# Performance work log

Hardware: AMD Instinct MI355X
Metric: run time of the kernel (lower is better)

Reference implementation:

```python
import jax, jax.numpy as jnp
import numpy as np

CH = 256            # channels
IN_C = CH // 2      # 128
INTER_C = CH // 16  # 16
NUM_POINTS = 32
BN_EPS = 1e-5


def conv1x1(x, W, b=None):
    # x: [B,C,H,W], W: [O,C]
    y = jnp.einsum('oc,bchw->bohw', W, x)
    if b is not None:
        y = y + b[None, :, None, None]
    return y


def bilinear_sample(feat, sx, sy):
    """feat [B,C,H,W]; sx,sy [B,N,P] continuous index coords; border padding."""
    B, C, H, W = feat.shape
    x0f = jnp.floor(sx)
    y0f = jnp.floor(sy)
    wx = sx - x0f
    wy = sy - y0f
    x0 = jnp.clip(x0f.astype(jnp.int32), 0, W - 1)
    x1 = jnp.clip(x0f.astype(jnp.int32) + 1, 0, W - 1)
    y0 = jnp.clip(y0f.astype(jnp.int32), 0, H - 1)
    y1 = jnp.clip(y0f.astype(jnp.int32) + 1, 0, H - 1)
    feat_f = feat.reshape(B, C, H * W).transpose(0, 2, 1)  # [B,HW,C]

    def gather(yi, xi):
        idx = (yi * W + xi).reshape(B, -1)  # [B,N*P]
        return jnp.take_along_axis(feat_f, idx[:, :, None], axis=1)  # [B,N*P,C]

    wxf = wx.reshape(B, -1, 1)
    wyf = wy.reshape(B, -1, 1)
    out = (gather(y0, x0) * (1 - wxf) * (1 - wyf)
           + gather(y0, x1) * wxf * (1 - wyf)
           + gather(y1, x0) * (1 - wxf) * wyf
           + gather(y1, x1) * wxf * wyf)
    N, P = sx.shape[1], sx.shape[2]
    return out.reshape(B, N, P, C)


def multi_scale_attention(qf, vf, Wq, bq, Wk, bk, Wv, bv, Woff, boff):
    # deformable-style point-sampling attention with NUM_POINTS samples per query
    B, _, H, W = qf.shape
    N = H * W
    q = conv1x1(qf, Wq, bq).reshape(B, INTER_C, N).transpose(0, 2, 1)  # [B,N,Ci]
    k = conv1x1(vf, Wk, bk)                                            # [B,Ci,H,W]
    v = conv1x1(vf, Wv, bv)                                            # [B,Cv,H,W]
    off = conv1x1(qf, Woff, boff).reshape(B, NUM_POINTS, 2, N)
    off = off.transpose(0, 3, 1, 2)                                    # [B,N,P,2] (dx,dy)
    ys, xs = jnp.meshgrid(jnp.arange(H, dtype=qf.dtype),
                          jnp.arange(W, dtype=qf.dtype), indexing='ij')
    sx = xs.reshape(-1)[None, :, None] + off[..., 0]                   # [B,N,P]
    sy = ys.reshape(-1)[None, :, None] + off[..., 1]
    k_s = bilinear_sample(k, sx, sy)                                   # [B,N,P,Ci]
    v_s = bilinear_sample(v, sx, sy)                                   # [B,N,P,Cv]
    logits = jnp.einsum('bnc,bnpc->bnp', q, k_s) / jnp.sqrt(jnp.asarray(INTER_C, qf.dtype))
    attn = jax.nn.softmax(logits, axis=-1)
    out = jnp.einsum('bnp,bnpc->bnc', attn, v_s)                       # [B,N,Cv]
    return out.transpose(0, 2, 1).reshape(B, -1, H, W)


def setup_inputs() -> dict:
    key = jax.random.key(0)
    ks = jax.random.split(key, 12)
    B, Hl, Wl, Hh, Wh = 2, 64, 64, 32, 32
    s = 0.02
    return {
        'low_feature': jax.random.normal(ks[0], (B, CH, Hl, Wl), jnp.float32),
        'high_feature': jax.random.normal(ks[1], (B, CH, Hh, Wh), jnp.float32),
        'W1': jax.random.normal(ks[2], (IN_C, 2 * CH), jnp.float32) * s,
        'b1': jnp.zeros((IN_C,), jnp.float32),
        'W2': jax.random.normal(ks[3], (IN_C, CH), jnp.float32) * s,
        'b2': jnp.zeros((IN_C,), jnp.float32),
        'Wq': jax.random.normal(ks[4], (INTER_C, IN_C), jnp.float32) * s,
        'bq': jnp.zeros((INTER_C,), jnp.float32),
        'Wk': jax.random.normal(ks[5], (INTER_C, IN_C), jnp.float32) * s,
        'bk': jnp.zeros((INTER_C,), jnp.float32),
        'Wv': jax.random.normal(ks[6], (IN_C, IN_C), jnp.float32) * s,
        'bv': jnp.zeros((IN_C,), jnp.float32),
        'Woff': jax.random.normal(ks[7], (2 * NUM_POINTS, IN_C), jnp.float32) * 0.5,
        'boff': jnp.zeros((2 * NUM_POINTS,), jnp.float32),
        'Wb': jax.random.normal(ks[8], (CH, IN_C + CH), jnp.float32) * s,
        'gamma': jnp.ones((CH,), jnp.float32),
        'beta': jnp.zeros((CH,), jnp.float32),
        'rmean': jnp.zeros((CH,), jnp.float32),
        'rvar': jnp.ones((CH,), jnp.float32),
    }


def reference(low_feature, high_feature, W1, b1, W2, b2, Wq, bq, Wk, bk,
              Wv, bv, Woff, boff, Wb, gamma, beta, rmean, rvar):
    B, _, Hl, Wl = low_feature.shape
    # F.interpolate(mode='bilinear', align_corners=False) == jax.image half-pixel bilinear
    high_up = jax.image.resize(high_feature, (B, CH, Hl, Wl), method='bilinear')
    query_feature = conv1x1(jnp.concatenate([high_up, low_feature], axis=1), W1, b1)
    value_feature = conv1x1(high_up, W2, b2)
    value_feature = multi_scale_attention(query_feature, value_feature,
                                          Wq, bq, Wk, bk, Wv, bv, Woff, boff)
    x = conv1x1(jnp.concatenate([value_feature, high_up], axis=1), Wb)
    # BatchNorm (eval form) + ReLU
    x = (x - rmean[None, :, None, None]) * jax.lax.rsqrt(rvar + BN_EPS)[None, :, None, None]
    x = x * gamma[None, :, None, None] + beta[None, :, None, None]
    return jax.nn.relu(x)
```

## Files before the change

### kernel.cpp

```cpp
#include <hip/hip_runtime.h>
#include <hip/hip_bf16.h>

#define NL 4096
#define HH 32
#define WH 32

typedef __attribute__((ext_vector_type(8))) short s8v;
typedef __attribute__((ext_vector_type(4))) short s4v;
typedef __attribute__((ext_vector_type(4))) float f32x4;

static __device__ inline unsigned short f2bf(float x) {
  __hip_bfloat16 h = __float2bfloat16(x);
  return *reinterpret_cast<unsigned short*>(&h);
}
static __device__ inline float bfbits2f(unsigned int lo16) {
  unsigned int u = lo16 << 16;
  return *reinterpret_cast<float*>(&u);
}

__global__ __launch_bounds__(256) void convert_weights_k(
    const float* __restrict__ w1, const float* __restrict__ w2,
    const float* __restrict__ wq, const float* __restrict__ woff,
    const float* __restrict__ wk, const float* __restrict__ wv,
    const float* __restrict__ wb, short* __restrict__ dst) {
  int i = blockIdx.x * 256 + threadIdx.x;
  const float* src; int off;
  if      (i <  65536) { src = w1;   off = 0; }
  else if (i <  98304) { src = w2;   off = 65536; }
  else if (i < 100352) { src = wq;   off = 98304; }
  else if (i < 108544) { src = woff; off = 100352; }
  else if (i < 110592) { src = wk;   off = 108544; }
  else if (i < 126976) { src = wv;   off = 110592; }
  else if (i < 225280) { src = wb;   off = 126976; }
  else return;
  dst[i] = (short)f2bf(src[i - off]);
}

__global__ __launch_bounds__(256) void k1_fused(
    const float* __restrict__ low, const float* __restrict__ high,
    const short* __restrict__ wc,
    const float* __restrict__ b1, const float* __restrict__ b2,
    const float* __restrict__ bq, const float* __restrict__ boff,
    const float* __restrict__ bk, const float* __restrict__ bv,
    short* __restrict__ xh, float* __restrict__ q_t, float* __restrict__ k_t,
    float* __restrict__ off_t, short* __restrict__ v_t) {
  __shared__ short xin_s[16 * 520];
  __shared__ short qf_s[16 * 136];
  __shared__ short vf_s[16 * 136];
  const int tid = threadIdx.x;
  const int pix0 = blockIdx.x * 16;
  const int b = pix0 >> 12;
  const int n0 = pix0 & (NL - 1);

  {
    const int nl = tid & 15, cg = tid >> 4;
    const int n = n0 + nl;
    const int y = n >> 6, x = n & 63;
    float sx = x * 0.5f - 0.25f;
    float sy = y * 0.5f - 0.25f;
    float x0f = floorf(sx), y0f = floorf(sy);
    float wx = sx - x0f, wy = sy - y0f;
    int x0i = (int)x0f, y0i = (int)y0f;
    int x0c = min(WH - 1, max(0, x0i)), x1c = min(WH - 1, max(0, x0i + 1));
    int y0c = min(HH - 1, max(0, y0i)), y1c = min(HH - 1, max(0, y0i + 1));
    float w00 = (1.f - wy) * (1.f - wx), w01 = (1.f - wy) * wx;
    float w10 = wy * (1.f - wx),         w11 = wy * wx;
#pragma unroll
    for (int i = 0; i < 16; i++) {
      int c = cg * 16 + i;
      const float* f = high + (size_t)(b * 256 + c) * (HH * WH);
      float v = w00 * f[y0c * WH + x0c] + w01 * f[y0c * WH + x1c]
              + w10 * f[y1c * WH + x0c] + w11 * f[y1c * WH + x1c];
      xin_s[nl * 520 + c] = (short)f2bf(v);
      xin_s[nl * 520 + 256 + c] =
          (short)f2bf(low[(size_t)(b * 256 + c) * NL + n]);
    }
  }
  __syncthreads();

  {
    const int r = tid >> 4, c0 = (tid & 15) * 16;
    s8v v0 = *(const s8v*)(xin_s + r * 520 + c0);
    s8v v1 = *(const s8v*)(xin_s + r * 520 + c0 + 8);
    *(s8v*)(xh + (size_t)(pix0 + r) * 256 + c0) = v0;
    *(s8v*)(xh + (size_t)(pix0 + r) * 256 + c0 + 8) = v1;
  }

  const int wave = tid >> 6, lane = tid & 63;
  const int quad = lane >> 4, id = lane & 15;

  {
    f32x4 acc0 = (f32x4){0.f, 0.f, 0.f, 0.f};
    f32x4 acc1 = (f32x4){0.f, 0.f, 0.f, 0.f};
    const short* a0 = wc + (size_t)(wave * 32 + id) * 512 + quad * 8;
    const short* a1 = a0 + 16 * 512;
    const short* bp = xin_s + id * 520 + quad * 8;
#pragma unroll
    for (int kk = 0; kk < 512; kk += 32) {
      s8v bf = *(const s8v*)(bp + kk);
      acc0 = __builtin_amdgcn_mfma_f32_16x16x32_bf16(*(const s8v*)(a0 + kk), bf, acc0, 0, 0, 0);
      acc1 = __builtin_amdgcn_mfma_f32_16x16x32_bf16(*(const s8v*)(a1 + kk), bf, acc1, 0, 0, 0);
    }
    int m0 = wave * 32 + quad * 4;
    s4v o0, o1;
#pragma unroll
    for (int r = 0; r < 4; r++) {
      o0[r] = (short)f2bf(acc0[r] + b1[m0 + r]);
      o1[r] = (short)f2bf(acc1[r] + b1[m0 + 16 + r]);
    }
    *(s4v*)(qf_s + id * 136 + m0) = o0;
    *(s4v*)(qf_s + id * 136 + m0 + 16) = o1;
  }

  {
    f32x4 acc0 = (f32x4){0.f, 0.f, 0.f, 0.f};
    f32x4 acc1 = (f32x4){0.f, 0.f, 0.f, 0.f};
    const short* a0 = wc + 65536 + (size_t)(wave * 32 + id) * 256 + quad * 8;
    const short* a1 = a0 + 16 * 256;
    const short* bp = xin_s + id * 520 + quad * 8;
#pragma unroll
    for (int kk = 0; kk < 256; kk += 32) {
      s8v bf = *(const s8v*)(bp + kk);
      acc0 = __builtin_amdgcn_mfma_f32_16x16x32_bf16(*(const s8v*)(a0 + kk), bf, acc0, 0, 0, 0);
      acc1 = __builtin_amdgcn_mfma_f32_16x16x32_bf16(*(const s8v*)(a1 + kk), bf, acc1, 0, 0, 0);
    }
    int m0 = wave * 32 + quad * 4;
    s4v o0, o1;
#pragma unroll
    for (int r = 0; r < 4; r++) {
      o0[r] = (short)f2bf(acc0[r] + b2[m0 + r]);
      o1[r] = (short)f2bf(acc1[r] + b2[m0 + 16 + r]);
    }
    *(s4v*)(vf_s + id * 136 + m0) = o0;
    *(s4v*)(vf_s + id * 136 + m0 + 16) = o1;
  }
  __syncthreads();

  for (int f = wave; f < 14; f += 4) {
    const short* ap = wc + 98304 + (size_t)(f * 16 + id) * 128 + quad * 8;
    const short* bp = (f < 5 ? qf_s : vf_s) + id * 136 + quad * 8;
    f32x4 acc = (f32x4){0.f, 0.f, 0.f, 0.f};
#pragma unroll
    for (int kk = 0; kk < 128; kk += 32)
      acc = __builtin_amdgcn_mfma_f32_16x16x32_bf16(
          *(const s8v*)(ap + kk), *(const s8v*)(bp + kk), acc, 0, 0, 0);
    const int pix = pix0 + id;
    const int mq = quad * 4;
    if (f == 0) {
      f32x4 v;
#pragma unroll
      for (int r = 0; r < 4; r++) v[r] = acc[r] + bq[mq + r];
      *(f32x4*)(q_t + (size_t)pix * 16 + mq) = v;
    } else if (f < 5) {
      int m = (f - 1) * 16 + mq;
      f32x4 v;
#pragma unroll
      for (int r = 0; r < 4; r++) v[r] = acc[r] + boff[m + r];
      *(f32x4*)(off_t + (size_t)pix * 64 + m) = v;
    } else if (f == 5) {
      f32x4 v;
#pragma unroll
      for (int r = 0; r < 4; r++) v[r] = acc[r] + bk[mq + r];
      *(f32x4*)(k_t + (size_t)pix * 16 + mq) = v;
    } else {
      int m = (f - 6) * 16 + mq;
      s4v o;
#pragma unroll
      for (int r = 0; r < 4; r++) o[r] = (short)f2bf(acc[r] + bv[m + r]);
      *(s4v*)(v_t + (size_t)pix * 128 + m) = o;
    }
  }
}

__global__ __launch_bounds__(1024, 2) void k2_fused(
    const float* __restrict__ q_t, const float* __restrict__ k_t,
    const short* __restrict__ v_t, const float* __restrict__ off_t,
    const short* __restrict__ xh, const short* __restrict__ wb,
    const float* __restrict__ gamma, const float* __restrict__ beta,
    const float* __restrict__ rmean, const float* __restrict__ rvar,
    float* __restrict__ out) {
  __shared__ float s_w[16][32][4];
  __shared__ int   s_i[16][32][4];
  __shared__ short attn_s[16 * 136];
  const int tid = threadIdx.x;
  const int wave = tid >> 6, lane = tid & 63;
  const int pix0 = blockIdx.x * 16;

  {
    const int qidx = pix0 + wave;
    const int b = qidx >> 12;
    const int n = qidx & (NL - 1);
    const int qy = n >> 6, qx = n & 63;

    const float* qp = q_t + (size_t)qidx * 16;
    float qreg[16];
#pragma unroll
    for (int i = 0; i < 16; i += 4) {
      float4 t = *(const float4*)(qp + i);
      qreg[i] = t.x; qreg[i + 1] = t.y; qreg[i + 2] = t.z; qreg[i + 3] = t.w;
    }

    const int pt = lane >> 1, h = lane & 1;
    float2 dxy = *(const float2*)(off_t + (size_t)qidx * 64 + 2 * pt);
    float sx = (float)qx + dxy.x;
    float sy = (float)qy + dxy.y;
    float x0f = floorf(sx), y0f = floorf(sy);
    float wx = sx - x0f, wy = sy - y0f;
    int x0i = (int)x0f, y0i = (int)y0f;
    int x0 = min(63, max(0, x0i)), x1 = min(63, max(0, x0i + 1));
    int y0 = min(63, max(0, y0i)), y1 = min(63, max(0, y0i + 1));

    int   yr  = h ? y1 : y0;
    float wyr = h ? wy : (1.f - wy);
    int   pa = yr * 64 + x0, pb = yr * 64 + x1;
    float wa = wyr * (1.f - wx), wb_ = wyr * wx;

    const float* kb = k_t + (size_t)b * NL * 16;
    float da = 0.f, db = 0.f;
    {
      const float* ka = kb + (size_t)pa * 16;
      const float* kc = kb + (size_t)pb * 16;
#pragma unroll
      for (int i = 0; i < 16; i += 4) {
        float4 a4 = *(const float4*)(ka + i);
        float4 c4 = *(const float4*)(kc + i);
        da = fmaf(qreg[i], a4.x, da); da = fmaf(qreg[i + 1], a4.y, da);
        da = fmaf(qreg[i + 2], a4.z, da); da = fmaf(qreg[i + 3], a4.w, da);
        db = fmaf(qreg[i], c4.x, db); db = fmaf(qreg[i + 1], c4.y, db);
        db = fmaf(qreg[i + 2], c4.z, db); db = fmaf(qreg[i + 3], c4.w, db);
      }
    }
    float part = wa * da + wb_ * db;
    part += __shfl_xor(part, 1, 64);
    float logit = part * 0.25f;

    float m = logit;
#pragma unroll
    for (int s = 32; s > 0; s >>= 1) m = fmaxf(m, __shfl_xor(m, s, 64));
    float e = __expf(logit - m);
    float ssum = e;
#pragma unroll
    for (int s = 32; s > 0; s >>= 1) ssum += __shfl_xor(ssum, s, 64);
    float a = e * 2.f / ssum;

    s_w[wave][pt][2 * h + 0] = a * wa;
    s_w[wave][pt][2 * h + 1] = a * wb_;
    s_i[wave][pt][2 * h + 0] = pa;
    s_i[wave][pt][2 * h + 1] = pb;

    const int t = lane >> 4, chunk = lane & 15;
    const short* vb = v_t + (size_t)b * NL * 128 + chunk * 8;
    float o[8];
#pragma unroll
    for (int j = 0; j < 8; j++) o[j] = 0.f;
#pragma unroll
    for (int pp = 0; pp < 32; pp++) {
      float w_ = s_w[wave][pp][t];
      int  pix = s_i[wave][pp][t];
      uint4 u = *(const uint4*)(vb + (size_t)pix * 128);
      o[0] = fmaf(w_, bfbits2f(u.x & 0xffffu), o[0]);
      o[1] = fmaf(w_, bfbits2f(u.x >> 16),     o[1]);
      o[2] = fmaf(w_, bfbits2f(u.y & 0xffffu), o[2]);
      o[3] = fmaf(w_, bfbits2f(u.y >> 16),     o[3]);
      o[4] = fmaf(w_, bfbits2f(u.z & 0xffffu), o[4]);
      o[5] = fmaf(w_, bfbits2f(u.z >> 16),     o[5]);
      o[6] = fmaf(w_, bfbits2f(u.w & 0xffffu), o[6]);
      o[7] = fmaf(w_, bfbits2f(u.w >> 16),     o[7]);
    }
#pragma unroll
    for (int j = 0; j < 8; j++) {
      o[j] += __shfl_xor(o[j], 16, 64);
      o[j] += __shfl_xor(o[j], 32, 64);
    }
    if (t == 0) {
      uint4 pk;
      pk.x = (unsigned)f2bf(o[0]) | ((unsigned)f2bf(o[1]) << 16);
      pk.y = (unsigned)f2bf(o[2]) | ((unsigned)f2bf(o[3]) << 16);
      pk.z = (unsigned)f2bf(o[4]) | ((unsigned)f2bf(o[5]) << 16);
      pk.w = (unsigned)f2bf(o[6]) | ((unsigned)f2bf(o[7]) << 16);
      *(uint4*)(attn_s + wave * 136 + chunk * 8) = pk;
    }
  }
  __syncthreads();

  {
    const int quad = lane >> 4, id = lane & 15;
    const int m0 = wave * 16;
    const int pix = pix0 + id;

    f32x4 acc = (f32x4){0.f, 0.f, 0.f, 0.f};
    const short* ap = wb + (size_t)(m0 + id) * 384 + quad * 8;
    const short* bs = attn_s + id * 136 + quad * 8;
    const short* bg = xh + (size_t)pix * 256 + quad * 8;
#pragma unroll
    for (int k = 0; k < 4; k++)
      acc = __builtin_amdgcn_mfma_f32_16x16x32_bf16(
          *(const s8v*)(ap + k * 32), *(const s8v*)(bs + k * 32), acc, 0, 0, 0);
#pragma unroll
    for (int k = 0; k < 8; k++)
      acc = __builtin_amdgcn_mfma_f32_16x16x32_bf16(
          *(const s8v*)(ap + 128 + k * 32), *(const s8v*)(bg + k * 32), acc, 0, 0, 0);

    const int bb = pix >> 12, nlow = pix & (NL - 1);
    const int mbase = m0 + quad * 4;
#pragma unroll
    for (int r = 0; r < 4; r++) {
      int o = mbase + r;
      float s  = gamma[o] * rsqrtf(rvar[o] + 1e-5f);
      float sh = beta[o] - rmean[o] * s;
      out[((size_t)bb * 256 + o) * NL + nlow] = fmaxf(fmaf(acc[r], s, sh), 0.f);
    }
  }
}

extern "C" void kernel_launch(void* const* d_in, const int* in_sizes, int n_in,
                              void* d_out, int out_size, void* d_ws, size_t ws_size,
                              hipStream_t stream) {
  const float* low   = (const float*)d_in[0];
  const float* high  = (const float*)d_in[1];
  const float* W1    = (const float*)d_in[2];
  const float* b1    = (const float*)d_in[3];
  const float* W2    = (const float*)d_in[4];
  const float* b2    = (const float*)d_in[5];
  const float* Wq    = (const float*)d_in[6];
  const float* bq    = (const float*)d_in[7];
  const float* Wk    = (const float*)d_in[8];
  const float* bk    = (const float*)d_in[9];
  const float* Wv    = (const float*)d_in[10];
  const float* bv    = (const float*)d_in[11];
  const float* Woff  = (const float*)d_in[12];
  const float* boff  = (const float*)d_in[13];
  const float* Wb    = (const float*)d_in[14];
  const float* gamma = (const float*)d_in[15];
  const float* beta  = (const float*)d_in[16];
  const float* rmean = (const float*)d_in[17];
  const float* rvar  = (const float*)d_in[18];
  float* out = (float*)d_out;

  short* ws    = (short*)d_ws;
  short* xh    = ws;
  short* v_t   = xh + 2097152;
  short* wc    = v_t + 1048576;
  float* q_t   = (float*)(wc + 225280);
  float* k_t   = q_t + 131072;
  float* off_t = k_t + 131072;

  convert_weights_k<<<880, 256, 0, stream>>>(W1, W2, Wq, Woff, Wk, Wv, Wb, wc);
  k1_fused<<<512, 256, 0, stream>>>(low, high, wc, b1, b2, bq, boff, bk, bv,
                                    xh, q_t, k_t, off_t, v_t);
  k2_fused<<<512, 1024, 0, stream>>>(q_t, k_t, v_t, off_t, xh, wc + 126976,
                                     gamma, beta, rmean, rvar, out);
}
```

Before: 155.9 us.

## Vectorize weight conversion, widen k1 blocks, swizzle workgroups, pack LDS sample table

Weight conversion now handles four elements per thread with float4 loads, so it needs a quarter of the blocks. k1 runs 512 threads per block, and each wave computes one 16-row MFMA tile instead of two, which doubles wave-level parallelism per block. Both main kernels remap block indices with an XCD-style swizzle. k2 packs sample weights and indices into one float2 LDS table and writes the output with nontemporal stores. These changes aim to cut launch and latency overheads and to improve cache locality, at the cost of more threads per block in k1.

Measured after the change: 152.5 us. -2.2%, faster.

```diff
diff --git a/kernel.cpp b/kernel.cpp
--- a/kernel.cpp
+++ b/kernel.cpp
@@ -16,6 +16,10 @@
 static __device__ inline float bfbits2f(unsigned int lo16) {
   unsigned int u = lo16 << 16;
   return *reinterpret_cast<float*>(&u);
+}
+
+static __device__ inline int swizzle_wg(int b) {
+  return ((b & 7) << 6) | (b >> 3);
 }
 
 __global__ __launch_bounds__(256) void convert_weights_k(
@@ -23,7 +27,7 @@
     const float* __restrict__ wq, const float* __restrict__ woff,
     const float* __restrict__ wk, const float* __restrict__ wv,
     const float* __restrict__ wb, short* __restrict__ dst) {
-  int i = blockIdx.x * 256 + threadIdx.x;
+  int i = (blockIdx.x * 256 + threadIdx.x) * 4;
   const float* src; int off;
   if      (i <  65536) { src = w1;   off = 0; }
   else if (i <  98304) { src = w2;   off = 65536; }
@@ -33,10 +37,14 @@
   else if (i < 126976) { src = wv;   off = 110592; }
   else if (i < 225280) { src = wb;   off = 126976; }
   else return;
-  dst[i] = (short)f2bf(src[i - off]);
-}
-
-__global__ __launch_bounds__(256) void k1_fused(
+  float4 v = *(const float4*)(src + (i - off));
+  s4v o;
+  o[0] = (short)f2bf(v.x); o[1] = (short)f2bf(v.y);
+  o[2] = (short)f2bf(v.z); o[3] = (short)f2bf(v.w);
+  *(s4v*)(dst + i) = o;
+}
+
+__global__ __launch_bounds__(512, 4) void k1_fused(
     const float* __restrict__ low, const float* __restrict__ high,
     const short* __restrict__ wc,
     const float* __restrict__ b1, const float* __restrict__ b2,
@@ -48,7 +56,8 @@
   __shared__ short qf_s[16 * 136];
   __shared__ short vf_s[16 * 136];
   const int tid = threadIdx.x;
-  const int pix0 = blockIdx.x * 16;
+  const int wg = swizzle_wg(blockIdx.x);
+  const int pix0 = wg * 16;
   const int b = pix0 >> 12;
   const int n0 = pix0 & (NL - 1);
 
@@ -66,8 +75,8 @@
     float w00 = (1.f - wy) * (1.f - wx), w01 = (1.f - wy) * wx;
     float w10 = wy * (1.f - wx),         w11 = wy * wx;
 #pragma unroll
-    for (int i = 0; i < 16; i++) {
-      int c = cg * 16 + i;
+    for (int i = 0; i < 8; i++) {
+      int c = cg * 8 + i;
       const float* f = high + (size_t)(b * 256 + c) * (HH * WH);
       float v = w00 * f[y0c * WH + x0c] + w01 * f[y0c * WH + x1c]
               + w10 * f[y1c * WH + x0c] + w11 * f[y1c * WH + x1c];
@@ -79,64 +88,46 @@
   __syncthreads();
 
   {
-    const int r = tid >> 4, c0 = (tid & 15) * 16;
+    const int r = tid >> 5, c0 = (tid & 31) * 8;
     s8v v0 = *(const s8v*)(xin_s + r * 520 + c0);
-    s8v v1 = *(const s8v*)(xin_s + r * 520 + c0 + 8);
     *(s8v*)(xh + (size_t)(pix0 + r) * 256 + c0) = v0;
-    *(s8v*)(xh + (size_t)(pix0 + r) * 256 + c0 + 8) = v1;
   }
 
   const int wave = tid >> 6, lane = tid & 63;
   const int quad = lane >> 4, id = lane & 15;
 
   {
-    f32x4 acc0 = (f32x4){0.f, 0.f, 0.f, 0.f};
-    f32x4 acc1 = (f32x4){0.f, 0.f, 0.f, 0.f};
-    const short* a0 = wc + (size_t)(wave * 32 + id) * 512 + quad * 8;
-    const short* a1 = a0 + 16 * 512;
+    f32x4 acc = (f32x4){0.f, 0.f, 0.f, 0.f};
+    const short* a0 = wc + (size_t)(wave * 16 + id) * 512 + quad * 8;
     const short* bp = xin_s + id * 520 + quad * 8;
 #pragma unroll
-    for (int kk = 0; kk < 512; kk += 32) {
-      s8v bf = *(const s8v*)(bp + kk);
-      acc0 = __builtin_amdgcn_mfma_f32_16x16x32_bf16(*(const s8v*)(a0 + kk), bf, acc0, 0, 0, 0);
-      acc1 = __builtin_amdgcn_mfma_f32_16x16x32_bf16(*(const s8v*)(a1 + kk), bf, acc1, 0, 0, 0);
-    }
-    int m0 = wave * 32 + quad * 4;
-    s4v o0, o1;
-#pragma unroll
-    for (int r = 0; r < 4; r++) {
-      o0[r] = (short)f2bf(acc0[r] + b1[m0 + r]);
-      o1[r] = (short)f2bf(acc1[r] + b1[m0 + 16 + r]);
-    }
+    for (int kk = 0; kk < 512; kk += 32)
+      acc = __builtin_amdgcn_mfma_f32_16x16x32_bf16(
+          *(const s8v*)(a0 + kk), *(const s8v*)(bp + kk), acc, 0, 0, 0);
+    int m0 = wave * 16 + quad * 4;
+    s4v o0;
+#pragma unroll
+    for (int r = 0; r < 4; r++) o0[r] = (short)f2bf(acc[r] + b1[m0 + r]);
     *(s4v*)(qf_s + id * 136 + m0) = o0;
-    *(s4v*)(qf_s + id * 136 + m0 + 16) = o1;
-  }
-
-  {
-    f32x4 acc0 = (f32x4){0.f, 0.f, 0.f, 0.f};
-    f32x4 acc1 = (f32x4){0.f, 0.f, 0.f, 0.f};
-    const short* a0 = wc + 65536 + (size_t)(wave * 32 + id) * 256 + quad * 8;
-    const short* a1 = a0 + 16 * 256;
+  }
+
+  {
+    f32x4 acc = (f32x4){0.f, 0.f, 0.f, 0.f};
+    const short* a0 = wc + 65536 + (size_t)(wave * 16 + id) * 256 + quad * 8;
     const short* bp = xin_s + id * 520 + quad * 8;
 #pragma unroll
-    for (int kk = 0; kk < 256; kk += 32) {
-      s8v bf = *(const s8v*)(bp + kk);
-      acc0 = __builtin_amdgcn_mfma_f32_16x16x32_bf16(*(const s8v*)(a0 + kk), bf, acc0, 0, 0, 0);
-      acc1 = __builtin_amdgcn_mfma_f32_16x16x32_bf16(*(const s8v*)(a1 + kk), bf, acc1, 0, 0, 0);
-    }
-    int m0 = wave * 32 + quad * 4;
-    s4v o0, o1;
-#pragma unroll
-    for (int r = 0; r < 4; r++) {
-      o0[r] = (short)f2bf(acc0[r] + b2[m0 + r]);
-      o1[r] = (short)f2bf(acc1[r] + b2[m0 + 16 + r]);
-    }
+    for (int kk = 0; kk < 256; kk += 32)
+      acc = __builtin_amdgcn_mfma_f32_16x16x32_bf16(
+          *(const s8v*)(a0 + kk), *(const s8v*)(bp + kk), acc, 0, 0, 0);
+    int m0 = wave * 16 + quad * 4;
+    s4v o0;
+#pragma unroll
+    for (int r = 0; r < 4; r++) o0[r] = (short)f2bf(acc[r] + b2[m0 + r]);
     *(s4v*)(vf_s + id * 136 + m0) = o0;
-    *(s4v*)(vf_s + id * 136 + m0 + 16) = o1;
   }
   __syncthreads();
 
-  for (int f = wave; f < 14; f += 4) {
+  for (int f = wave; f < 14; f += 8) {
     const short* ap = wc + 98304 + (size_t)(f * 16 + id) * 128 + quad * 8;
     const short* bp = (f < 5 ? qf_s : vf_s) + id * 136 + quad * 8;
     f32x4 acc = (f32x4){0.f, 0.f, 0.f, 0.f};
@@ -179,12 +170,12 @@
     const float* __restrict__ gamma, const float* __restrict__ beta,
     const float* __restrict__ rmean, const float* __restrict__ rvar,
     float* __restrict__ out) {
-  __shared__ float s_w[16][32][4];
-  __shared__ int   s_i[16][32][4];
+  __shared__ float2 s_wi[16][32][4];
   __shared__ short attn_s[16 * 136];
   const int tid = threadIdx.x;
   const int wave = tid >> 6, lane = tid & 63;
-  const int pix0 = blockIdx.x * 16;
+  const int wg = swizzle_wg(blockIdx.x);
+  const int pix0 = wg * 16;
 
   {
     const int qidx = pix0 + wave;
@@ -243,10 +234,8 @@
     for (int s = 32; s > 0; s >>= 1) ssum += __shfl_xor(ssum, s, 64);
     float a = e * 2.f / ssum;
 
-    s_w[wave][pt][2 * h + 0] = a * wa;
-    s_w[wave][pt][2 * h + 1] = a * wb_;
-    s_i[wave][pt][2 * h + 0] = pa;
-    s_i[wave][pt][2 * h + 1] = pb;
+    s_wi[wave][pt][2 * h + 0] = make_float2(a * wa,  __int_as_float(pa));
+    s_wi[wave][pt][2 * h + 1] = make_float2(a * wb_, __int_as_float(pb));
 
     const int t = lane >> 4, chunk = lane & 15;
     const short* vb = v_t + (size_t)b * NL * 128 + chunk * 8;
@@ -255,8 +244,9 @@
     for (int j = 0; j < 8; j++) o[j] = 0.f;
 #pragma unroll
     for (int pp = 0; pp < 32; pp++) {
-      float w_ = s_w[wave][pp][t];
-      int  pix = s_i[wave][pp][t];
+      float2 wi = s_wi[wave][pp][t];
+      float w_ = wi.x;
+      int  pix = __float_as_int(wi.y);
       uint4 u = *(const uint4*)(vb + (size_t)pix * 128);
       o[0] = fmaf(w_, bfbits2f(u.x & 0xffffu), o[0]);
       o[1] = fmaf(w_, bfbits2f(u.x >> 16),     o[1]);
@@ -308,7 +298,8 @@
       int o = mbase + r;
       float s  = gamma[o] * rsqrtf(rvar[o] + 1e-5f);
       float sh = beta[o] - rmean[o] * s;
-      out[((size_t)bb * 256 + o) * NL + nlow] = fmaxf(fmaf(acc[r], s, sh), 0.f);
+      __builtin_nontemporal_store(fmaxf(fmaf(acc[r], s, sh), 0.f),
+                                  &out[((size_t)bb * 256 + o) * NL + nlow]);
     }
   }
 }
@@ -345,8 +336,8 @@
   float* k_t   = q_t + 131072;
   float* off_t = k_t + 131072;
 
-  convert_weights_k<<<880, 256, 0, stream>>>(W1, W2, Wq, Woff, Wk, Wv, Wb, wc);
-  k1_fused<<<512, 256, 0, stream>>>(low, high, wc, b1, b2, bq, boff, bk, bv,
+  convert_weights_k<<<220, 256, 0, stream>>>(W1, W2, Wq, Woff, Wk, Wv, Wb, wc);
+  k1_fused<<<512, 512, 0, stream>>>(low, high, wc, b1, b2, bq, boff, bk, bv,
                                     xh, q_t, k_t, off_t, v_t);
   k2_fused<<<512, 1024, 0, stream>>>(q_t, k_t, v_t, off_t, xh, wc + 126976,
                                      gamma, beta, rmean, rvar, out);
```
